# Kernel optimization log

Hardware: AMD Instinct MI355X
Metric: run time of the kernel (lower is better)

Reference implementation:

```python
import jax, jax.numpy as jnp
import numpy as np

NUM_HEADS = 6
LOCAL_KS = 3


def setup_inputs() -> dict:
    key = jax.random.key(0)
    k1, k2, k3, k4 = jax.random.split(key, 4)
    B, N, C = 8, 1024, 384
    x = jax.random.normal(k1, (B, N, C), dtype=jnp.float32)
    qkv_w = jax.random.normal(k2, (3 * C, C), dtype=jnp.float32) * (C ** -0.5)
    proj_w = jax.random.normal(k3, (C, C), dtype=jnp.float32) * (C ** -0.5)
    proj_b = jax.random.normal(k4, (C,), dtype=jnp.float32) * 0.01
    return {"x": x, "qkv_w": qkv_w, "proj_w": proj_w, "proj_b": proj_b}


def reference(x, qkv_w, proj_w, proj_b):
    B, N, C = x.shape
    H = NUM_HEADS
    hd = C // H
    scale = hd ** -0.5
    half = LOCAL_KS // 2

    # qkv projection: [B,N,3C] -> q,k,v each [B,H,N,hd]
    qkv = (x @ qkv_w.T).reshape(B, N, 3, H, hd).transpose(2, 0, 3, 1, 4)
    q, k, v = qkv[0], qkv[1], qkv[2]

    # dense scores with banded local mask (clamped window == |i-j| <= half)
    attn = jnp.einsum('bhqd,bhkd->bhqk', q, k) * scale
    idx = jnp.arange(N)
    mask = jnp.abs(idx[:, None] - idx[None, :]) > half  # True -> masked out
    attn = jnp.where(mask, -jnp.inf, attn)
    p = jax.nn.softmax(attn, axis=-1)

    # AV then merge heads: [B,N,C]
    out = jnp.einsum('bhqk,bhkd->bqhd', p, v).reshape(B, N, C)
    return out @ proj_w.T + proj_b
```

## Files before the change

### kernel.cpp

```cpp
#include <hip/hip_runtime.h>
#include <hip/hip_bf16.h>
#include <math.h>

#define C_DIM 384
#define NHEADS 6
#define HD 64
#define BATCH 8
#define NSEQ 1024
#define M_ROWS (BATCH * NSEQ)

typedef __attribute__((ext_vector_type(4))) float f32x4;
typedef __attribute__((ext_vector_type(8))) short s16x8;

__device__ __forceinline__ float bf2f(short u) {
  return __uint_as_float(((unsigned)(unsigned short)u) << 16);
}
__device__ __forceinline__ short f2bf(float f) {
  __hip_bfloat16 h = __float2bfloat16(f);
  return *reinterpret_cast<short*>(&h);
}
__device__ __forceinline__ s16x8 cvt8(float4 a, float4 b) {
  s16x8 r;
  r[0] = f2bf(a.x); r[1] = f2bf(a.y); r[2] = f2bf(a.z); r[3] = f2bf(a.w);
  r[4] = f2bf(b.x); r[5] = f2bf(b.y); r[6] = f2bf(b.z); r[7] = f2bf(b.w);
  return r;
}

__device__ __forceinline__ void gload_lds16(const void* g, void* l) {
  __builtin_amdgcn_global_load_lds(
      (const __attribute__((address_space(1))) unsigned int*)g,
      (__attribute__((address_space(3))) unsigned int*)l, 16, 0, 0);
}

__device__ __forceinline__ void wait_vm0() {
  asm volatile("s_waitcnt vmcnt(0)" ::: "memory");
}
__device__ __forceinline__ void lgkm0() {
  asm volatile("s_waitcnt lgkmcnt(0)" ::: "memory");
}
__device__ __forceinline__ void bar() {
  __builtin_amdgcn_sched_barrier(0);
  __builtin_amdgcn_s_barrier();
  __builtin_amdgcn_sched_barrier(0);
}

__global__ __launch_bounds__(512) void gemm1_rs(
    const float* __restrict__ A, const float* __restrict__ W,
    __hip_bfloat16* __restrict__ outp, int M, int N, int K) {
  __shared__ __align__(16) __hip_bfloat16 As[2][128 * 32];
  __shared__ __align__(16) __hip_bfloat16 Bs[2][128 * 32];

  const int tid = threadIdx.x;
  const int nwg = gridDim.x * gridDim.y;
  const int bid0 = blockIdx.y * gridDim.x + blockIdx.x;
  const int cpx = nwg >> 3;
  const int wg = (bid0 & 7) * cpx + (bid0 >> 3);
  const int bx = wg % gridDim.x;
  const int by = wg / gridDim.x;

  const int lane = tid & 63;
  const int wave = tid >> 6;
  const int wr = (wave >> 2) * 64;
  const int wc = (wave & 3) * 32;
  const int rowBase = by * 128;
  const int colBase = bx * 128;
  const int l16 = lane & 15;
  const int lk8 = (lane >> 4) * 8;
  const int lr4 = (lane >> 4) * 4;

  const int sr = tid >> 2;
  const int sc = (tid & 3) * 8;
  const float* aSrc = A + (size_t)(rowBase + sr) * K + sc;
  const float* bSrc = W + (size_t)(colBase + sr) * K + sc;

  f32x4 acc[4][2] = {};
  float4 aL[2], bL[2];

  auto loadRegs = [&](int kt) {
    const float4* ap = (const float4*)(aSrc + kt * 32);
    aL[0] = ap[0]; aL[1] = ap[1];
    const float4* bp = (const float4*)(bSrc + kt * 32);
    bL[0] = bp[0]; bL[1] = bp[1];
  };

  loadRegs(0);
  const int nkt = K >> 5;
  for (int kt = 0; kt < nkt; ++kt) {
    const int cur = kt & 1;
    wait_vm0();
    __builtin_amdgcn_sched_barrier(0);
    *(s16x8*)&As[cur][sr * 32 + sc] = cvt8(aL[0], aL[1]);
    *(s16x8*)&Bs[cur][sr * 32 + sc] = cvt8(bL[0], bL[1]);
    if (kt + 1 < nkt) loadRegs(kt + 1);
    lgkm0();
    bar();

    s16x8 af[4], bfr[2];
#pragma unroll
    for (int m = 0; m < 4; ++m)
      af[m] = *(const s16x8*)(&As[cur][(wr + m * 16 + l16) * 32 + lk8]);
#pragma unroll
    for (int n = 0; n < 2; ++n)
      bfr[n] = *(const s16x8*)(&Bs[cur][(wc + n * 16 + l16) * 32 + lk8]);
#pragma unroll
    for (int m = 0; m < 4; ++m)
#pragma unroll
      for (int n = 0; n < 2; ++n)
        acc[m][n] = __builtin_amdgcn_mfma_f32_16x16x32_bf16(
            af[m], bfr[n], acc[m][n], 0, 0, 0);
    bar();
  }

#pragma unroll
  for (int m = 0; m < 4; ++m) {
    int rb = rowBase + wr + m * 16 + lr4;
#pragma unroll
    for (int n = 0; n < 2; ++n) {
      int cb = colBase + wc + n * 16 + l16;
#pragma unroll
      for (int j = 0; j < 4; ++j)
        outp[(size_t)(rb + j) * N + cb] = __float2bfloat16(acc[m][n][j]);
    }
  }
}

__global__ __launch_bounds__(256) void gemm2_mix(
    const __hip_bfloat16* __restrict__ A, const float* __restrict__ W,
    const float* __restrict__ bias, float* __restrict__ outp,
    int M, int N, int K) {
  __shared__ __align__(16) __hip_bfloat16 As[2][128 * 32];
  __shared__ __align__(16) __hip_bfloat16 Bs[2][64 * 32];

  const int tid = threadIdx.x;
  const int nwg = gridDim.x * gridDim.y;
  const int bid0 = blockIdx.y * gridDim.x + blockIdx.x;
  const int cpx = nwg >> 3;
  const int wg = (bid0 & 7) * cpx + (bid0 >> 3);
  const int bx = wg % gridDim.x;
  const int by = wg / gridDim.x;

  const int lane = tid & 63;
  const int wave = tid >> 6;
  const int wr = (wave >> 1) * 64;
  const int wc = (wave & 1) * 32;
  const int rowBase = by * 128;
  const int colBase = bx * 64;
  const int l16 = lane & 15;
  const int lk8 = (lane >> 4) * 8;
  const int lr4 = (lane >> 4) * 4;

  const int sr = tid >> 2;
  const int sc = (tid & 3) * 8;
  const float* bSrc = W + (size_t)(colBase + sr) * K + sc;

  f32x4 acc[4][2] = {};
  float4 bL[2];

  auto stageA = [&](int kt, int buf) {
#pragma unroll
    for (int i = 0; i < 2; ++i) {
      int c = tid + i * 256;
      int r = c >> 2, cc = (c & 3) * 8;
      gload_lds16(A + (size_t)(rowBase + r) * K + kt * 32 + cc, &As[buf][c * 8]);
    }
  };
  auto loadB = [&](int kt) {
    const float4* bp = (const float4*)(bSrc + kt * 32);
    bL[0] = bp[0]; bL[1] = bp[1];
  };

  stageA(0, 0);
  loadB(0);
  const int nkt = K >> 5;
  for (int kt = 0; kt < nkt; ++kt) {
    const int cur = kt & 1;
    wait_vm0();
    __builtin_amdgcn_sched_barrier(0);
    *(s16x8*)&Bs[cur][sr * 32 + sc] = cvt8(bL[0], bL[1]);
    if (kt + 1 < nkt) {
      stageA(kt + 1, cur ^ 1);
      loadB(kt + 1);
    }
    lgkm0();
    bar();

    s16x8 af[4], bfr[2];
#pragma unroll
    for (int m = 0; m < 4; ++m)
      af[m] = *(const s16x8*)(&As[cur][(wr + m * 16 + l16) * 32 + lk8]);
#pragma unroll
    for (int n = 0; n < 2; ++n)
      bfr[n] = *(const s16x8*)(&Bs[cur][(wc + n * 16 + l16) * 32 + lk8]);
#pragma unroll
    for (int m = 0; m < 4; ++m)
#pragma unroll
      for (int n = 0; n < 2; ++n)
        acc[m][n] = __builtin_amdgcn_mfma_f32_16x16x32_bf16(
            af[m], bfr[n], acc[m][n], 0, 0, 0);
    bar();
  }

#pragma unroll
  for (int m = 0; m < 4; ++m) {
    int rb = rowBase + wr + m * 16 + lr4;
#pragma unroll
    for (int n = 0; n < 2; ++n) {
      int cb = colBase + wc + n * 16 + l16;
      float bv = bias[cb];
#pragma unroll
      for (int j = 0; j < 4; ++j)
        outp[(size_t)(rb + j) * N + cb] = acc[m][n][j] + bv;
    }
  }
}

__global__ __launch_bounds__(256) void local_attn_v3(
    const __hip_bfloat16* __restrict__ qkv, __hip_bfloat16* __restrict__ attn_out) {
  __shared__ __align__(16) ushort lds[24832];
  const int QOFF = 0;
  const int KOFF = 8192;
  const int VOFF = 8192 + 8320;

  const int tid = threadIdx.x;
  const int mb = blockIdx.x & 63;
  const int h  = blockIdx.x >> 6;
  const int rb = mb * 128;
  const int b  = rb >> 10;
  const int n0 = rb & 1023;
  const int RS = 3 * C_DIM;

#pragma unroll
  for (int i = 0; i < 4; ++i) {
    int s = i * 256 + tid;
    int r = s >> 3;
    int jg = (s & 7) ^ (r & 7);
    gload_lds16(qkv + (size_t)(rb + r) * RS + h * HD + jg * 8,
                lds + QOFF + s * 8);
  }
#pragma unroll
  for (int i = 0; i < 5; ++i) {
    int s = i * 256 + tid;
    if (s < 1040) {
      int r = s >> 3;
      int jg = (s & 7) ^ (r & 7);
      int nl = n0 + r - 1;
      nl = nl < 0 ? 0 : (nl > 1023 ? 1023 : nl);
      size_t row = (size_t)(b << 10) + nl;
      gload_lds16(qkv + row * RS + C_DIM + h * HD + jg * 8, lds + KOFF + s * 8);
      gload_lds16(qkv + row * RS + 2 * C_DIM + h * HD + jg * 8, lds + VOFF + s * 8);
    }
  }
  __syncthreads();

  const int r = tid >> 1;
  const int half = tid & 1;
  const int jbase = half * 4;
  const int n = n0 + r;

  float qf[32];
#pragma unroll
  for (int c = 0; c < 4; ++c) {
    int slot = r * 8 + ((jbase + c) ^ (r & 7));
    s16x8 v = *(const s16x8*)(lds + QOFF + slot * 8);
#pragma unroll
    for (int e = 0; e < 8; ++e) qf[c * 8 + e] = bf2f(v[e]);
  }

  float s3[3];
#pragma unroll
  for (int jj = 0; jj < 3; ++jj) {
    int krow = r + jj;
    float acc = 0.f;
#pragma unroll
    for (int c = 0; c < 4; ++c) {
      int slot = krow * 8 + ((jbase + c) ^ (krow & 7));
      s16x8 v = *(const s16x8*)(lds + KOFF + slot * 8);
#pragma unroll
      for (int e = 0; e < 8; ++e) acc += qf[c * 8 + e] * bf2f(v[e]);
    }
    acc += __shfl_xor(acc, 1);
    s3[jj] = ((unsigned)(n + jj - 1) < (unsigned)NSEQ) ? acc * 0.125f : -1e30f;
  }

  float mx = fmaxf(s3[0], fmaxf(s3[1], s3[2]));
  float p0 = __expf(s3[0] - mx);
  float p1 = __expf(s3[1] - mx);
  float p2 = __expf(s3[2] - mx);
  float inv = 1.f / (p0 + p1 + p2);
  float p[3] = {p0 * inv, p1 * inv, p2 * inv};

  float of[32] = {};
#pragma unroll
  for (int jj = 0; jj < 3; ++jj) {
    int krow = r + jj;
    float pw = p[jj];
#pragma unroll
    for (int c = 0; c < 4; ++c) {
      int slot = krow * 8 + ((jbase + c) ^ (krow & 7));
      s16x8 v = *(const s16x8*)(lds + VOFF + slot * 8);
#pragma unroll
      for (int e = 0; e < 8; ++e) of[c * 8 + e] += pw * bf2f(v[e]);
    }
  }

#pragma unroll
  for (int c = 0; c < 4; ++c) {
    s16x8 o;
#pragma unroll
    for (int e = 0; e < 8; ++e) o[e] = f2bf(of[c * 8 + e]);
    *(s16x8*)(attn_out + (size_t)(rb + r) * C_DIM + h * HD + jbase * 8 + c * 8) = o;
  }
}

extern "C" void kernel_launch(void* const* d_in, const int* in_sizes, int n_in,
                              void* d_out, int out_size, void* d_ws, size_t ws_size,
                              hipStream_t stream) {
  const float* x      = (const float*)d_in[0];
  const float* qkv_w  = (const float*)d_in[1];
  const float* proj_w = (const float*)d_in[2];
  const float* proj_b = (const float*)d_in[3];
  float* out = (float*)d_out;

  __hip_bfloat16* qkv_bf  = (__hip_bfloat16*)d_ws;
  __hip_bfloat16* attn_bf = qkv_bf + (size_t)M_ROWS * 3 * C_DIM;

  gemm1_rs<<<dim3(9, 64), 512, 0, stream>>>(
      x, qkv_w, qkv_bf, M_ROWS, 3 * C_DIM, C_DIM);

  local_attn_v3<<<64 * NHEADS, 256, 0, stream>>>(qkv_bf, attn_bf);

  gemm2_mix<<<dim3(6, 64), 256, 0, stream>>>(
      attn_bf, proj_w, proj_b, out, M_ROWS, C_DIM, C_DIM);
}
```

Baseline: 42.85 us.

## Pad LDS rows, enlarge per-wave tiles, restructure GEMM double-buffer pipelining

```diff
diff --git a/kernel.cpp b/kernel.cpp
--- a/kernel.cpp
+++ b/kernel.cpp
@@ -8,6 +8,7 @@
 #define BATCH 8
 #define NSEQ 1024
 #define M_ROWS (BATCH * NSEQ)
+#define LDP 40
 
 typedef __attribute__((ext_vector_type(4))) float f32x4;
 typedef __attribute__((ext_vector_type(8))) short s16x8;
@@ -44,11 +45,11 @@
   __builtin_amdgcn_sched_barrier(0);
 }
 
-__global__ __launch_bounds__(512) void gemm1_rs(
+__global__ __launch_bounds__(256) void gemm1_rs(
     const float* __restrict__ A, const float* __restrict__ W,
     __hip_bfloat16* __restrict__ outp, int M, int N, int K) {
-  __shared__ __align__(16) __hip_bfloat16 As[2][128 * 32];
-  __shared__ __align__(16) __hip_bfloat16 Bs[2][128 * 32];
+  __shared__ __align__(16) __hip_bfloat16 As[2][128 * LDP];
+  __shared__ __align__(16) __hip_bfloat16 Bs[2][128 * LDP];
 
   const int tid = threadIdx.x;
   const int nwg = gridDim.x * gridDim.y;
@@ -60,62 +61,72 @@
 
   const int lane = tid & 63;
   const int wave = tid >> 6;
-  const int wr = (wave >> 2) * 64;
-  const int wc = (wave & 3) * 32;
+  const int wr = (wave >> 1) * 64;
+  const int wc = (wave & 1) * 64;
   const int rowBase = by * 128;
   const int colBase = bx * 128;
   const int l16 = lane & 15;
   const int lk8 = (lane >> 4) * 8;
   const int lr4 = (lane >> 4) * 4;
 
-  const int sr = tid >> 2;
-  const int sc = (tid & 3) * 8;
+  const int sr = tid >> 1;
+  const int sc = (tid & 1) * 16;
   const float* aSrc = A + (size_t)(rowBase + sr) * K + sc;
   const float* bSrc = W + (size_t)(colBase + sr) * K + sc;
 
-  f32x4 acc[4][2] = {};
-  float4 aL[2], bL[2];
+  f32x4 acc[4][4] = {};
+  float4 aL[4], bL[4];
 
   auto loadRegs = [&](int kt) {
     const float4* ap = (const float4*)(aSrc + kt * 32);
-    aL[0] = ap[0]; aL[1] = ap[1];
+    aL[0] = ap[0]; aL[1] = ap[1]; aL[2] = ap[2]; aL[3] = ap[3];
     const float4* bp = (const float4*)(bSrc + kt * 32);
-    bL[0] = bp[0]; bL[1] = bp[1];
+    bL[0] = bp[0]; bL[1] = bp[1]; bL[2] = bp[2]; bL[3] = bp[3];
   };
-
+  auto writeLds = [&](int buf) {
+    *(s16x8*)&As[buf][sr * LDP + sc]     = cvt8(aL[0], aL[1]);
+    *(s16x8*)&As[buf][sr * LDP + sc + 8] = cvt8(aL[2], aL[3]);
+    *(s16x8*)&Bs[buf][sr * LDP + sc]     = cvt8(bL[0], bL[1]);
+    *(s16x8*)&Bs[buf][sr * LDP + sc + 8] = cvt8(bL[2], bL[3]);
+  };
+
+  const int nkt = K >> 5;
   loadRegs(0);
-  const int nkt = K >> 5;
+  wait_vm0();
+  writeLds(0);
+  loadRegs(1);
+  lgkm0();
+  bar();
+
   for (int kt = 0; kt < nkt; ++kt) {
     const int cur = kt & 1;
-    wait_vm0();
-    __builtin_amdgcn_sched_barrier(0);
-    *(s16x8*)&As[cur][sr * 32 + sc] = cvt8(aL[0], aL[1]);
-    *(s16x8*)&Bs[cur][sr * 32 + sc] = cvt8(bL[0], bL[1]);
-    if (kt + 1 < nkt) loadRegs(kt + 1);
+    if (kt + 1 < nkt) {
+      wait_vm0();
+      writeLds(cur ^ 1);
+      if (kt + 2 < nkt) loadRegs(kt + 2);
+    }
+    s16x8 af[4], bfr[4];
+#pragma unroll
+    for (int m = 0; m < 4; ++m)
+      af[m] = *(const s16x8*)(&As[cur][(wr + m * 16 + l16) * LDP + lk8]);
+#pragma unroll
+    for (int n = 0; n < 4; ++n)
+      bfr[n] = *(const s16x8*)(&Bs[cur][(wc + n * 16 + l16) * LDP + lk8]);
+#pragma unroll
+    for (int m = 0; m < 4; ++m)
+#pragma unroll
+      for (int n = 0; n < 4; ++n)
+        acc[m][n] = __builtin_amdgcn_mfma_f32_16x16x32_bf16(
+            af[m], bfr[n], acc[m][n], 0, 0, 0);
     lgkm0();
     bar();
-
-    s16x8 af[4], bfr[2];
-#pragma unroll
-    for (int m = 0; m < 4; ++m)
-      af[m] = *(const s16x8*)(&As[cur][(wr + m * 16 + l16) * 32 + lk8]);
-#pragma unroll
-    for (int n = 0; n < 2; ++n)
-      bfr[n] = *(const s16x8*)(&Bs[cur][(wc + n * 16 + l16) * 32 + lk8]);
-#pragma unroll
-    for (int m = 0; m < 4; ++m)
-#pragma unroll
-      for (int n = 0; n < 2; ++n)
-        acc[m][n] = __builtin_amdgcn_mfma_f32_16x16x32_bf16(
-            af[m], bfr[n], acc[m][n], 0, 0, 0);
-    bar();
   }
 
 #pragma unroll
   for (int m = 0; m < 4; ++m) {
     int rb = rowBase + wr + m * 16 + lr4;
 #pragma unroll
-    for (int n = 0; n < 2; ++n) {
+    for (int n = 0; n < 4; ++n) {
       int cb = colBase + wc + n * 16 + l16;
 #pragma unroll
       for (int j = 0; j < 4; ++j)
@@ -128,8 +139,8 @@
     const __hip_bfloat16* __restrict__ A, const float* __restrict__ W,
     const float* __restrict__ bias, float* __restrict__ outp,
     int M, int N, int K) {
-  __shared__ __align__(16) __hip_bfloat16 As[2][128 * 32];
-  __shared__ __align__(16) __hip_bfloat16 Bs[2][64 * 32];
+  __shared__ __align__(16) __hip_bfloat16 As[2][128 * LDP];
+  __shared__ __align__(16) __hip_bfloat16 Bs[2][64 * LDP];
 
   const int tid = threadIdx.x;
   const int nwg = gridDim.x * gridDim.y;
@@ -149,54 +160,58 @@
   const int lk8 = (lane >> 4) * 8;
   const int lr4 = (lane >> 4) * 4;
 
-  const int sr = tid >> 2;
-  const int sc = (tid & 3) * 8;
-  const float* bSrc = W + (size_t)(colBase + sr) * K + sc;
+  const int srA = tid >> 1;
+  const int scA = (tid & 1) * 16;
+  const __hip_bfloat16* aSrc = A + (size_t)(rowBase + srA) * K + scA;
+  const int srB = tid >> 2;
+  const int scB = (tid & 3) * 8;
+  const float* bSrc = W + (size_t)(colBase + srB) * K + scB;
 
   f32x4 acc[4][2] = {};
+  s16x8 aL[2];
   float4 bL[2];
 
-  auto stageA = [&](int kt, int buf) {
-#pragma unroll
-    for (int i = 0; i < 2; ++i) {
-      int c = tid + i * 256;
-      int r = c >> 2, cc = (c & 3) * 8;
-      gload_lds16(A + (size_t)(rowBase + r) * K + kt * 32 + cc, &As[buf][c * 8]);
-    }
-  };
-  auto loadB = [&](int kt) {
+  auto loadRegs = [&](int kt) {
+    const s16x8* ap = (const s16x8*)(aSrc + kt * 32);
+    aL[0] = ap[0]; aL[1] = ap[1];
     const float4* bp = (const float4*)(bSrc + kt * 32);
     bL[0] = bp[0]; bL[1] = bp[1];
   };
-
-  stageA(0, 0);
-  loadB(0);
+  auto writeLds = [&](int buf) {
+    *(s16x8*)&As[buf][srA * LDP + scA]     = aL[0];
+    *(s16x8*)&As[buf][srA * LDP + scA + 8] = aL[1];
+    *(s16x8*)&Bs[buf][srB * LDP + scB]     = cvt8(bL[0], bL[1]);
+  };
+
   const int nkt = K >> 5;
+  loadRegs(0);
+  wait_vm0();
+  writeLds(0);
+  loadRegs(1);
+  lgkm0();
+  bar();
+
   for (int kt = 0; kt < nkt; ++kt) {
     const int cur = kt & 1;
-    wait_vm0();
-    __builtin_amdgcn_sched_barrier(0);
-    *(s16x8*)&Bs[cur][sr * 32 + sc] = cvt8(bL[0], bL[1]);
     if (kt + 1 < nkt) {
-      stageA(kt + 1, cur ^ 1);
-      loadB(kt + 1);
-    }
-    lgkm0();
-    bar();
-
+      wait_vm0();
+      writeLds(cur ^ 1);
+      if (kt + 2 < nkt) loadRegs(kt + 2);
+    }
     s16x8 af[4], bfr[2];
 #pragma unroll
     for (int m = 0; m < 4; ++m)
-      af[m] = *(const s16x8*)(&As[cur][(wr + m * 16 + l16) * 32 + lk8]);
+      af[m] = *(const s16x8*)(&As[cur][(wr + m * 16 + l16) * LDP + lk8]);
 #pragma unroll
     for (int n = 0; n < 2; ++n)
-      bfr[n] = *(const s16x8*)(&Bs[cur][(wc + n * 16 + l16) * 32 + lk8]);
+      bfr[n] = *(const s16x8*)(&Bs[cur][(wc + n * 16 + l16) * LDP + lk8]);
 #pragma unroll
     for (int m = 0; m < 4; ++m)
 #pragma unroll
       for (int n = 0; n < 2; ++n)
         acc[m][n] = __builtin_amdgcn_mfma_f32_16x16x32_bf16(
             af[m], bfr[n], acc[m][n], 0, 0, 0);
+    lgkm0();
     bar();
   }
 
@@ -324,7 +339,7 @@
   __hip_bfloat16* qkv_bf  = (__hip_bfloat16*)d_ws;
   __hip_bfloat16* attn_bf = qkv_bf + (size_t)M_ROWS * 3 * C_DIM;
 
-  gemm1_rs<<<dim3(9, 64), 512, 0, stream>>>(
+  gemm1_rs<<<dim3(9, 64), 256, 0, stream>>>(
       x, qkv_w, qkv_bf, M_ROWS, 3 * C_DIM, C_DIM);
 
   local_attn_v3<<<64 * NHEADS, 256, 0, stream>>>(qkv_bf, attn_bf);
```

New measurement: 46.88 us. 9.4% more time.

## Fuse QKV projection with banded local attention in one kernel

Applied to the files above, without the earlier changes.

```diff
diff --git a/kernel.cpp b/kernel.cpp
--- a/kernel.cpp
+++ b/kernel.cpp
@@ -8,6 +8,7 @@
 #define BATCH 8
 #define NSEQ 1024
 #define M_ROWS (BATCH * NSEQ)
+#define LDP 40
 
 typedef __attribute__((ext_vector_type(4))) float f32x4;
 typedef __attribute__((ext_vector_type(8))) short s16x8;
@@ -44,82 +45,189 @@
   __builtin_amdgcn_sched_barrier(0);
 }
 
-__global__ __launch_bounds__(512) void gemm1_rs(
-    const float* __restrict__ A, const float* __restrict__ W,
-    __hip_bfloat16* __restrict__ outp, int M, int N, int K) {
-  __shared__ __align__(16) __hip_bfloat16 As[2][128 * 32];
-  __shared__ __align__(16) __hip_bfloat16 Bs[2][128 * 32];
+__global__ __launch_bounds__(512) void qkv_attn(
+    const float* __restrict__ x, const float* __restrict__ W,
+    __hip_bfloat16* __restrict__ attn_out) {
+  __shared__ __align__(16) ushort lds[25856];
+  const int BSO = 10240;
+  const int QOFF = 0, KOFF = 8192, VOFF = 16512;
+  float* fh = (float*)lds + 12800;
 
   const int tid = threadIdx.x;
-  const int nwg = gridDim.x * gridDim.y;
-  const int bid0 = blockIdx.y * gridDim.x + blockIdx.x;
-  const int cpx = nwg >> 3;
-  const int wg = (bid0 & 7) * cpx + (bid0 >> 3);
-  const int bx = wg % gridDim.x;
-  const int by = wg / gridDim.x;
+  const int g = blockIdx.x;
+  const int h = (g >> 3) % 6;
+  const int panel = (g / 48) * 8 + (g & 7);
+  const int rb = panel << 7;
+  const int b = rb >> 10;
+  const int n0 = rb & 1023;
 
   const int lane = tid & 63;
   const int wave = tid >> 6;
   const int wr = (wave >> 2) * 64;
-  const int wc = (wave & 3) * 32;
-  const int rowBase = by * 128;
-  const int colBase = bx * 128;
+  const int wc = (wave & 3) * 48;
   const int l16 = lane & 15;
   const int lk8 = (lane >> 4) * 8;
   const int lr4 = (lane >> 4) * 4;
 
   const int sr = tid >> 2;
   const int sc = (tid & 3) * 8;
-  const float* aSrc = A + (size_t)(rowBase + sr) * K + sc;
-  const float* bSrc = W + (size_t)(colBase + sr) * K + sc;
-
-  f32x4 acc[4][2] = {};
-  float4 aL[2], bL[2];
+  const float* aSrc = x + (size_t)(rb + sr) * C_DIM + sc;
+  const int rB = tid >> 1;
+  const int cB = (tid & 1) * 16;
+  const int strip = rB >> 6;
+  const float* bSrc = W + (size_t)(strip * C_DIM + h * HD + (rB & 63)) * C_DIM + cB;
+  const int hsr = tid >> 3;
+  const int hsc = (tid & 7) * 4;
+  const int hg0 = b * NSEQ + (n0 > 0 ? n0 - 1 : 0);
+  const int hg1 = b * NSEQ + (n0 + 128 < NSEQ ? n0 + 128 : NSEQ - 1);
+  const float* hSrc = x + (size_t)(hsr ? hg1 : hg0) * C_DIM + hsc;
+  const int hrow = tid >> 7;
+  const int hcol = tid & 127;
+
+  f32x4 acc[4][3] = {};
+  float hacc = 0.f;
+  float4 aL[2], bL[4], hL;
 
   auto loadRegs = [&](int kt) {
     const float4* ap = (const float4*)(aSrc + kt * 32);
     aL[0] = ap[0]; aL[1] = ap[1];
-    const float4* bp = (const float4*)(bSrc + kt * 32);
-    bL[0] = bp[0]; bL[1] = bp[1];
+    if (tid < 384) {
+      const float4* bp = (const float4*)(bSrc + kt * 32);
+      bL[0] = bp[0]; bL[1] = bp[1]; bL[2] = bp[2]; bL[3] = bp[3];
+    }
+    if (tid < 16) hL = *(const float4*)(hSrc + kt * 32);
   };
+  auto writeLds = [&](int buf) {
+    *(s16x8*)(lds + buf * 5120 + sr * LDP + sc) = cvt8(aL[0], aL[1]);
+    if (tid < 384) {
+      *(s16x8*)(lds + BSO + buf * 7680 + rB * LDP + cB)     = cvt8(bL[0], bL[1]);
+      *(s16x8*)(lds + BSO + buf * 7680 + rB * LDP + cB + 8) = cvt8(bL[2], bL[3]);
+    }
+    if (tid < 16) *(float4*)(fh + buf * 64 + hsr * 32 + hsc) = hL;
+  };
 
   loadRegs(0);
-  const int nkt = K >> 5;
+  const int nkt = C_DIM >> 5;
   for (int kt = 0; kt < nkt; ++kt) {
     const int cur = kt & 1;
     wait_vm0();
     __builtin_amdgcn_sched_barrier(0);
-    *(s16x8*)&As[cur][sr * 32 + sc] = cvt8(aL[0], aL[1]);
-    *(s16x8*)&Bs[cur][sr * 32 + sc] = cvt8(bL[0], bL[1]);
+    writeLds(cur);
     if (kt + 1 < nkt) loadRegs(kt + 1);
     lgkm0();
     bar();
 
-    s16x8 af[4], bfr[2];
+    s16x8 af[4], bfr[3];
 #pragma unroll
     for (int m = 0; m < 4; ++m)
-      af[m] = *(const s16x8*)(&As[cur][(wr + m * 16 + l16) * 32 + lk8]);
-#pragma unroll
-    for (int n = 0; n < 2; ++n)
-      bfr[n] = *(const s16x8*)(&Bs[cur][(wc + n * 16 + l16) * 32 + lk8]);
+      af[m] = *(const s16x8*)(lds + cur * 5120 + (wr + m * 16 + l16) * LDP + lk8);
+#pragma unroll
+    for (int n = 0; n < 3; ++n)
+      bfr[n] = *(const s16x8*)(lds + BSO + cur * 7680 + (wc + n * 16 + l16) * LDP + lk8);
 #pragma unroll
     for (int m = 0; m < 4; ++m)
 #pragma unroll
-      for (int n = 0; n < 2; ++n)
+      for (int n = 0; n < 3; ++n)
         acc[m][n] = __builtin_amdgcn_mfma_f32_16x16x32_bf16(
             af[m], bfr[n], acc[m][n], 0, 0, 0);
+
+    if (tid < 256) {
+      const ushort* brow = lds + BSO + cur * 7680 + (64 + hcol) * LDP;
+      const float* ah = fh + cur * 64 + hrow * 32;
+#pragma unroll
+      for (int kk = 0; kk < 4; ++kk) {
+        s16x8 bv = *(const s16x8*)(brow + kk * 8);
+#pragma unroll
+        for (int e = 0; e < 8; ++e)
+          hacc += ah[kk * 8 + e] * bf2f(bv[e]);
+      }
+    }
     bar();
   }
 
 #pragma unroll
   for (int m = 0; m < 4; ++m) {
-    int rb = rowBase + wr + m * 16 + lr4;
-#pragma unroll
-    for (int n = 0; n < 2; ++n) {
-      int cb = colBase + wc + n * 16 + l16;
-#pragma unroll
-      for (int j = 0; j < 4; ++j)
-        outp[(size_t)(rb + j) * N + cb] = __float2bfloat16(acc[m][n][j]);
+#pragma unroll
+    for (int n = 0; n < 3; ++n) {
+      int col = wc + n * 16 + l16;
+#pragma unroll
+      for (int j = 0; j < 4; ++j) {
+        int row = wr + m * 16 + lr4 + j;
+        short hv = f2bf(acc[m][n][j]);
+        int base, d, arow;
+        if (col < 64)       { base = QOFF; d = col;       arow = row; }
+        else if (col < 128) { base = KOFF; d = col - 64;  arow = row + 1; }
+        else                { base = VOFF; d = col - 128; arow = row + 1; }
+        lds[base + (arow * 8 + ((d >> 3) ^ (arow & 7))) * 8 + (d & 7)] = (ushort)hv;
+      }
+    }
+  }
+  if (tid < 256) {
+    int arow = hrow ? 129 : 0;
+    int base = (hcol < 64) ? KOFF : VOFF;
+    int d = (hcol < 64) ? hcol : hcol - 64;
+    lds[base + (arow * 8 + ((d >> 3) ^ (arow & 7))) * 8 + (d & 7)] = (ushort)f2bf(hacc);
+  }
+  __syncthreads();
+
+  if (tid < 256) {
+    const int r = tid >> 1;
+    const int half = tid & 1;
+    const int jbase = half * 4;
+    const int n = n0 + r;
+
+    float qf[32];
+#pragma unroll
+    for (int c = 0; c < 4; ++c) {
+      int slot = r * 8 + ((jbase + c) ^ (r & 7));
+      s16x8 v = *(const s16x8*)(lds + QOFF + slot * 8);
+#pragma unroll
+      for (int e = 0; e < 8; ++e) qf[c * 8 + e] = bf2f(v[e]);
+    }
+
+    float s3[3];
+#pragma unroll
+    for (int jj = 0; jj < 3; ++jj) {
+      int krow = r + jj;
+      float a = 0.f;
+#pragma unroll
+      for (int c = 0; c < 4; ++c) {
+        int slot = krow * 8 + ((jbase + c) ^ (krow & 7));
+        s16x8 v = *(const s16x8*)(lds + KOFF + slot * 8);
+#pragma unroll
+        for (int e = 0; e < 8; ++e) a += qf[c * 8 + e] * bf2f(v[e]);
+      }
+      a += __shfl_xor(a, 1);
+      s3[jj] = ((unsigned)(n + jj - 1) < (unsigned)NSEQ) ? a * 0.125f : -1e30f;
+    }
+
+    float mx = fmaxf(s3[0], fmaxf(s3[1], s3[2]));
+    float p0 = __expf(s3[0] - mx);
+    float p1 = __expf(s3[1] - mx);
+    float p2 = __expf(s3[2] - mx);
+    float inv = 1.f / (p0 + p1 + p2);
+    float p[3] = {p0 * inv, p1 * inv, p2 * inv};
+
+    float of[32] = {};
+#pragma unroll
+    for (int jj = 0; jj < 3; ++jj) {
+      int krow = r + jj;
+      float pw = p[jj];
+#pragma unroll
+      for (int c = 0; c < 4; ++c) {
+        int slot = krow * 8 + ((jbase + c) ^ (krow & 7));
+        s16x8 v = *(const s16x8*)(lds + VOFF + slot * 8);
+#pragma unroll
+        for (int e = 0; e < 8; ++e) of[c * 8 + e] += pw * bf2f(v[e]);
+      }
+    }
+
+#pragma unroll
+    for (int c = 0; c < 4; ++c) {
+      s16x8 o;
+#pragma unroll
+      for (int e = 0; e < 8; ++e) o[e] = f2bf(of[c * 8 + e]);
+      *(s16x8*)(attn_out + (size_t)(rb + r) * C_DIM + h * HD + jbase * 8 + c * 8) = o;
     }
   }
 }
@@ -214,104 +322,6 @@
   }
 }
 
-__global__ __launch_bounds__(256) void local_attn_v3(
-    const __hip_bfloat16* __restrict__ qkv, __hip_bfloat16* __restrict__ attn_out) {
-  __shared__ __align__(16) ushort lds[24832];
-  const int QOFF = 0;
-  const int KOFF = 8192;
-  const int VOFF = 8192 + 8320;
-
-  const int tid = threadIdx.x;
-  const int mb = blockIdx.x & 63;
-  const int h  = blockIdx.x >> 6;
-  const int rb = mb * 128;
-  const int b  = rb >> 10;
-  const int n0 = rb & 1023;
-  const int RS = 3 * C_DIM;
-
-#pragma unroll
-  for (int i = 0; i < 4; ++i) {
-    int s = i * 256 + tid;
-    int r = s >> 3;
-    int jg = (s & 7) ^ (r & 7);
-    gload_lds16(qkv + (size_t)(rb + r) * RS + h * HD + jg * 8,
-                lds + QOFF + s * 8);
-  }
-#pragma unroll
-  for (int i = 0; i < 5; ++i) {
-    int s = i * 256 + tid;
-    if (s < 1040) {
-      int r = s >> 3;
-      int jg = (s & 7) ^ (r & 7);
-      int nl = n0 + r - 1;
-      nl = nl < 0 ? 0 : (nl > 1023 ? 1023 : nl);
-      size_t row = (size_t)(b << 10) + nl;
-      gload_lds16(qkv + row * RS + C_DIM + h * HD + jg * 8, lds + KOFF + s * 8);
-      gload_lds16(qkv + row * RS + 2 * C_DIM + h * HD + jg * 8, lds + VOFF + s * 8);
-    }
-  }
-  __syncthreads();
-
-  const int r = tid >> 1;
-  const int half = tid & 1;
-  const int jbase = half * 4;
-  const int n = n0 + r;
-
-  float qf[32];
-#pragma unroll
-  for (int c = 0; c < 4; ++c) {
-    int slot = r * 8 + ((jbase + c) ^ (r & 7));
-    s16x8 v = *(const s16x8*)(lds + QOFF + slot * 8);
-#pragma unroll
-    for (int e = 0; e < 8; ++e) qf[c * 8 + e] = bf2f(v[e]);
-  }
-
-  float s3[3];
-#pragma unroll
-  for (int jj = 0; jj < 3; ++jj) {
-    int krow = r + jj;
-    float acc = 0.f;
-#pragma unroll
-    for (int c = 0; c < 4; ++c) {
-      int slot = krow * 8 + ((jbase + c) ^ (krow & 7));
-      s16x8 v = *(const s16x8*)(lds + KOFF + slot * 8);
-#pragma unroll
-      for (int e = 0; e < 8; ++e) acc += qf[c * 8 + e] * bf2f(v[e]);
-    }
-    acc += __shfl_xor(acc, 1);
-    s3[jj] = ((unsigned)(n + jj - 1) < (unsigned)NSEQ) ? acc * 0.125f : -1e30f;
-  }
-
-  float mx = fmaxf(s3[0], fmaxf(s3[1], s3[2]));
-  float p0 = __expf(s3[0] - mx);
-  float p1 = __expf(s3[1] - mx);
-  float p2 = __expf(s3[2] - mx);
-  float inv = 1.f / (p0 + p1 + p2);
-  float p[3] = {p0 * inv, p1 * inv, p2 * inv};
-
-  float of[32] = {};
-#pragma unroll
-  for (int jj = 0; jj < 3; ++jj) {
-    int krow = r + jj;
-    float pw = p[jj];
-#pragma unroll
-    for (int c = 0; c < 4; ++c) {
-      int slot = krow * 8 + ((jbase + c) ^ (krow & 7));
-      s16x8 v = *(const s16x8*)(lds + VOFF + slot * 8);
-#pragma unroll
-      for (int e = 0; e < 8; ++e) of[c * 8 + e] += pw * bf2f(v[e]);
-    }
-  }
-
-#pragma unroll
-  for (int c = 0; c < 4; ++c) {
-    s16x8 o;
-#pragma unroll
-    for (int e = 0; e < 8; ++e) o[e] = f2bf(of[c * 8 + e]);
-    *(s16x8*)(attn_out + (size_t)(rb + r) * C_DIM + h * HD + jbase * 8 + c * 8) = o;
-  }
-}
-
 extern "C" void kernel_launch(void* const* d_in, const int* in_sizes, int n_in,
                               void* d_out, int out_size, void* d_ws, size_t ws_size,
                               hipStream_t stream) {
@@ -321,13 +331,9 @@
   const float* proj_b = (const float*)d_in[3];
   float* out = (float*)d_out;
 
-  __hip_bfloat16* qkv_bf  = (__hip_bfloat16*)d_ws;
-  __hip_bfloat16* attn_bf = qkv_bf + (size_t)M_ROWS * 3 * C_DIM;
-
-  gemm1_rs<<<dim3(9, 64), 512, 0, stream>>>(
-      x, qkv_w, qkv_bf, M_ROWS, 3 * C_DIM, C_DIM);
-
-  local_attn_v3<<<64 * NHEADS, 256, 0, stream>>>(qkv_bf, attn_bf);
+  __hip_bfloat16* attn_bf = (__hip_bfloat16*)d_ws;
+
+  qkv_attn<<<384, 512, 0, stream>>>(x, qkv_w, attn_bf);
 
   gemm2_mix<<<dim3(6, 64), 256, 0, stream>>>(
       attn_bf, proj_w, proj_b, out, M_ROWS, C_DIM, C_DIM);
```

After: 46.02 us. 7.4% more time.
